# Kernel optimization log

Hardware: AMD Instinct MI355X
Metric: run time of the kernel (lower is better)

Reference implementation:

```python
import jax, jax.numpy as jnp
import numpy as np

B, S, D, H = 2, 2048, 1024, 16
DK = D // H


def setup_inputs() -> dict:
    key = jax.random.key(0)
    ks = jax.random.split(key, 12)
    k_init = 1.0 / np.sqrt(D)  # torch Linear-style uniform bound used in the module
    def lin(kw, kb):
        W = jax.random.uniform(kw, (D, D), jnp.float32, -k_init, k_init)
        b = jax.random.uniform(kb, (D,), jnp.float32, -k_init, k_init)
        return W, b
    Wq, bq = lin(ks[0], ks[1])
    Wk, bk = lin(ks[2], ks[3])
    Wv, bv = lin(ks[4], ks[5])
    Wo, bo = lin(ks[6], ks[7])
    query = jax.random.normal(ks[8], (B, S, D), jnp.float32)
    key_t = jax.random.normal(ks[9], (B, S, D), jnp.float32)
    value = jax.random.normal(ks[10], (B, S, D), jnp.float32)
    # causal mask: 1 where attention allowed, 0 where blocked
    mask = jnp.broadcast_to(jnp.tril(jnp.ones((S, S), jnp.int32)), (B, S, S))
    return {"query": query, "key": key_t, "value": value, "mask": mask,
            "Wq": Wq, "bq": bq, "Wk": Wk, "bk": bk, "Wv": Wv, "bv": bv,
            "Wo": Wo, "bo": bo}


def reference(query, key, value, mask, Wq, bq, Wk, bk, Wv, bv, Wo, bo):
    bs = query.shape[0]
    # projections: torch Linear computes x @ W.T + b
    def proj(x, W, b):
        y = x @ W.T + b                      # [B, S, D]
        return y.reshape(bs, -1, H, DK).transpose(0, 2, 1, 3)  # [B, H, S, DK]
    q = proj(query, Wq, bq)
    k = proj(key, Wk, bk)
    v = proj(value, Wv, bv)
    scale = 1.0 / np.sqrt(DK).astype(np.float32)
    scores = jnp.einsum('bhqd,bhkd->bhqk', q, k) * scale  # [B, H, S, S]
    scores = jnp.where(mask[:, None, :, :] == 0, jnp.float32(-1e9), scores)
    p_attn = jax.nn.softmax(scores, axis=-1)
    # dropout omitted (eval mode / deterministic reference)
    x = jnp.einsum('bhqk,bhkd->bhqd', p_attn, v)          # [B, H, S, DK]
    x = x.transpose(0, 2, 1, 3).reshape(bs, -1, D)        # [B, S, D]
    return x @ Wo.T + bo
```

## Files before the change

### kernel.cpp

```cpp
#include <hip/hip_runtime.h>
#include <hip/hip_bf16.h>
#include <math.h>

#define BB 2
#define SS 2048
#define DD 1024
#define HH 16
#define DKK 64
#define NT (BB * SS)
#define QBLK 128
#define NQT (SS / QBLK)

typedef __attribute__((ext_vector_type(8))) short short8;
typedef __attribute__((ext_vector_type(4))) float f32x4;

#define SWZ(r) ((((r) >> 3) ^ (r)) & 7)

__device__ __forceinline__ unsigned short f2b(float x) {
    __hip_bfloat16 h = __float2bfloat16(x);
    unsigned short u; __builtin_memcpy(&u, &h, 2); return u;
}

__device__ __forceinline__ f32x4 zero4() {
    f32x4 z; z[0] = 0.f; z[1] = 0.f; z[2] = 0.f; z[3] = 0.f; return z;
}

struct CastAll {
    const float* src[7];
    unsigned short* dst[7];
};

__global__ __launch_bounds__(256)
void cast_all(CastAll a) {
    const int tid0 = blockIdx.x * 256 + threadIdx.x;
    const int stride = gridDim.x * 256;
    #pragma unroll
    for (int s = 0; s < 7; ++s) {
        const int n4 = (s < 3) ? (NT * DD / 4) : (DD * DD / 4);
        const float* __restrict__ src = a.src[s];
        unsigned short* __restrict__ dst = a.dst[s];
        for (int i = tid0; i < n4; i += stride) {
            const float4 v = reinterpret_cast<const float4*>(src)[i];
            ushort4 o;
            o.x = f2b(v.x); o.y = f2b(v.y); o.z = f2b(v.z); o.w = f2b(v.w);
            reinterpret_cast<ushort4*>(dst)[i] = o;
        }
    }
}

template <typename OutT>
__device__ __forceinline__ void gemm_body(const unsigned short* __restrict__ A,
                                          const unsigned short* __restrict__ W,
                                          const float* __restrict__ bias,
                                          OutT* __restrict__ C,
                                          int bm, int bn, int N, int K) {
    __shared__ __align__(16) unsigned char sA[128 * 128];
    __shared__ __align__(16) unsigned char sB[128 * 128];

    const int tid = threadIdx.x;
    const int l = tid & 63;
    const int w = tid >> 6;
    const int wr = w >> 1, wc = w & 1;
    const int g = l >> 4, li = l & 15;
    const int lrow = l >> 3;
    const int lcol = (l & 7) * 8;

    f32x4 acc[4][4];
    #pragma unroll
    for (int i = 0; i < 4; ++i)
        #pragma unroll
        for (int jj = 0; jj < 4; ++jj) acc[i][jj] = zero4();

    for (int kt = 0; kt < K; kt += 64) {
        #pragma unroll
        for (int c = 0; c < 4; ++c) {
            const int row0 = w * 32 + c * 8;
            const unsigned short* gA = A + (size_t)(bm + row0 + lrow) * K + kt + lcol;
            __builtin_amdgcn_global_load_lds(
                (const __attribute__((address_space(1))) unsigned int*)gA,
                (__attribute__((address_space(3))) unsigned int*)&sA[row0 * 128],
                16, 0, 0);
            const unsigned short* gB = W + (size_t)(bn + row0 + lrow) * K + kt + lcol;
            __builtin_amdgcn_global_load_lds(
                (const __attribute__((address_space(1))) unsigned int*)gB,
                (__attribute__((address_space(3))) unsigned int*)&sB[row0 * 128],
                16, 0, 0);
        }
        __syncthreads();

        #pragma unroll
        for (int kb = 0; kb < 2; ++kb) {
            const int chb = (g + kb * 4) * 16;
            short8 af[4], bfr[4];
            #pragma unroll
            for (int mi = 0; mi < 4; ++mi)
                af[mi] = *reinterpret_cast<const short8*>(
                    &sA[(wr * 64 + mi * 16 + li) * 128 + chb]);
            #pragma unroll
            for (int ni = 0; ni < 4; ++ni)
                bfr[ni] = *reinterpret_cast<const short8*>(
                    &sB[(wc * 64 + ni * 16 + li) * 128 + chb]);
            #pragma unroll
            for (int mi = 0; mi < 4; ++mi)
                #pragma unroll
                for (int ni = 0; ni < 4; ++ni)
                    acc[mi][ni] = __builtin_amdgcn_mfma_f32_16x16x32_bf16(af[mi], bfr[ni], acc[mi][ni], 0, 0, 0);
        }
        __syncthreads();
    }

    #pragma unroll
    for (int ni = 0; ni < 4; ++ni) {
        const int col = bn + wc * 64 + ni * 16 + li;
        const float bv = bias[col];
        #pragma unroll
        for (int mi = 0; mi < 4; ++mi) {
            const int row0 = bm + wr * 64 + mi * 16 + g * 4;
            #pragma unroll
            for (int r = 0; r < 4; ++r) {
                const float v = acc[mi][ni][r] + bv;
                if constexpr (sizeof(OutT) == 2)
                    C[(size_t)(row0 + r) * N + col] = (OutT)f2b(v);
                else
                    C[(size_t)(row0 + r) * N + col] = (OutT)v;
            }
        }
    }
}

struct QKVArgs {
    const unsigned short* A[3];
    const unsigned short* W[3];
    const float* bias[3];
    unsigned short* C[3];
};

__global__ __launch_bounds__(256)
void gemm_qkv(QKVArgs args) {
    const int bid = blockIdx.x;
    const int i = (bid & 7) * 96 + (bid >> 3);
    const int z = i >> 8;
    const int rem = i & 255;
    const int by = rem >> 3, bx = rem & 7;
    gemm_body<unsigned short>(args.A[z], args.W[z], args.bias[z], args.C[z],
                              by * 128, bx * 128, DD, DD);
}

__global__ __launch_bounds__(256)
void gemm_out(const unsigned short* __restrict__ A, const unsigned short* __restrict__ W,
              const float* __restrict__ bias, float* __restrict__ C) {
    const int bid = blockIdx.x;
    const int i = (bid & 7) * 32 + (bid >> 3);
    const int by = i >> 3, bx = i & 7;
    gemm_body<float>(A, W, bias, C, by * 128, bx * 128, DD, DD);
}

__global__ __launch_bounds__(512)
void attn_mfma(const unsigned short* __restrict__ Q,
               const unsigned short* __restrict__ Kb,
               const unsigned short* __restrict__ Vb,
               unsigned short* __restrict__ X) {
    __shared__ __align__(16) unsigned char sK[64 * 128];
    __shared__ __align__(16) unsigned char sV[64 * 128];
    __shared__ __align__(16) unsigned char sP[8][16 * 128];

    const int bid = blockIdx.x;
    const int j = bid >> 3;
    const int pair = (bid & 7) * 4 + (j >> 4);
    const int qt = (NQT - 1) - (j & 15);
    const int b = pair >> 4, h = pair & 15;

    const int tid = threadIdx.x, l = tid & 63, w = tid >> 6;
    const int g = l >> 4, li = l & 15;
    const int tok0 = b * SS + qt * QBLK;
    const int col0 = h * DKK;
    const float scale = 0.125f;

    short8 qf[2];
    {
        const size_t qrow = (size_t)(tok0 + w * 16 + li) * DD + col0;
        qf[0] = *reinterpret_cast<const short8*>(&Q[qrow + g * 8]);
        qf[1] = *reinterpret_cast<const short8*>(&Q[qrow + 32 + g * 8]);
    }

    f32x4 accO[4];
    #pragma unroll
    for (int i = 0; i < 4; ++i) accO[i] = zero4();
    float m = -INFINITY, lsum = 0.f;
    const int qglob = qt * QBLK + w * 16 + li;
    const int qminw = qt * QBLK + w * 16;
    const int ktmax = 2 * qt + 1;

    for (int kt = 0; kt <= ktmax; ++kt) {
        const int ktok0 = b * SS + kt * 64;

        {
            const int row = tid >> 3, cj = tid & 7;
            const size_t gsrc = (size_t)(ktok0 + row) * DD + col0 + cj * 8;
            const short8 kv8 = *reinterpret_cast<const short8*>(&Kb[gsrc]);
            *reinterpret_cast<short8*>(&sK[row * 128 + ((cj ^ SWZ(row)) << 4)]) = kv8;
            const short8 vv8 = *reinterpret_cast<const short8*>(&Vb[gsrc]);
            #pragma unroll
            for (int jj = 0; jj < 8; ++jj) {
                const int d = cj * 8 + jj;
                *reinterpret_cast<unsigned short*>(
                    &sV[d * 128 + (((row >> 3) ^ SWZ(d)) << 4) + (row & 7) * 2]) =
                    (unsigned short)vv8[jj];
            }
        }
        __syncthreads();

        if (kt * 64 <= qminw + 15) {
            f32x4 accS[4];
            #pragma unroll
            for (int n0 = 0; n0 < 4; ++n0) accS[n0] = zero4();
            #pragma unroll
            for (int n0 = 0; n0 < 4; ++n0) {
                #pragma unroll
                for (int kb = 0; kb < 2; ++kb) {
                    const int row = n0 * 16 + li;
                    const int ch = g + kb * 4;
                    const short8 kf = *reinterpret_cast<const short8*>(
                        &sK[row * 128 + ((ch ^ SWZ(row)) << 4)]);
                    accS[n0] = __builtin_amdgcn_mfma_f32_16x16x32_bf16(kf, qf[kb], accS[n0], 0, 0, 0);
                }
            }

            const bool needMask = (kt * 64 + 63) > qminw;
            float s[16];
            float tmax = -INFINITY;
            #pragma unroll
            for (int n0 = 0; n0 < 4; ++n0)
                #pragma unroll
                for (int r = 0; r < 4; ++r) {
                    float v = accS[n0][r] * scale;
                    if (needMask) {
                        const int kv = kt * 64 + n0 * 16 + g * 4 + r;
                        if (kv > qglob) v = -1e30f;
                    }
                    s[n0 * 4 + r] = v;
                    tmax = fmaxf(tmax, v);
                }
            tmax = fmaxf(tmax, __shfl_xor(tmax, 16));
            tmax = fmaxf(tmax, __shfl_xor(tmax, 32));
            const float mnew = fmaxf(m, tmax);
            const float corr = __expf(m - mnew);
            float psum = 0.f;
            #pragma unroll
            for (int i = 0; i < 16; ++i) { s[i] = __expf(s[i] - mnew); psum += s[i]; }
            psum += __shfl_xor(psum, 16);
            psum += __shfl_xor(psum, 32);
            lsum = lsum * corr + psum;
            m = mnew;

            #pragma unroll
            for (int n0 = 0; n0 < 4; ++n0)
                #pragma unroll
                for (int r = 0; r < 4; ++r) {
                    const int kv = n0 * 16 + g * 4 + r;
                    *reinterpret_cast<unsigned short*>(
                        &sP[w][li * 128 + (((kv >> 3) ^ SWZ(li)) << 4) + (kv & 7) * 2]) =
                        f2b(s[n0 * 4 + r]);
                }

            float corr4[4];
            #pragma unroll
            for (int r = 0; r < 4; ++r) corr4[r] = __shfl(corr, (l & 48) | (g * 4 + r));
            #pragma unroll
            for (int n0d = 0; n0d < 4; ++n0d)
                #pragma unroll
                for (int r = 0; r < 4; ++r) accO[n0d][r] *= corr4[r];

            #pragma unroll
            for (int kb = 0; kb < 2; ++kb) {
                const int ch = g + kb * 4;
                const short8 pf = *reinterpret_cast<const short8*>(
                    &sP[w][li * 128 + ((ch ^ SWZ(li)) << 4)]);
                #pragma unroll
                for (int n0d = 0; n0d < 4; ++n0d) {
                    const int d = n0d * 16 + li;
                    const short8 vf = *reinterpret_cast<const short8*>(
                        &sV[d * 128 + ((ch ^ SWZ(d)) << 4)]);
                    accO[n0d] = __builtin_amdgcn_mfma_f32_16x16x32_bf16(pf, vf, accO[n0d], 0, 0, 0);
                }
            }
        }
        __syncthreads();
    }

    const float invl = 1.f / lsum;
    float inv4[4];
    #pragma unroll
    for (int r = 0; r < 4; ++r) inv4[r] = __shfl(invl, (l & 48) | (g * 4 + r));
    #pragma unroll
    for (int n0d = 0; n0d < 4; ++n0d)
        #pragma unroll
        for (int r = 0; r < 4; ++r) {
            const int row = tok0 + w * 16 + g * 4 + r;
            const int d = n0d * 16 + li;
            X[(size_t)row * DD + col0 + d] = f2b(accO[n0d][r] * inv4[r]);
        }
}

extern "C" void kernel_launch(void* const* d_in, const int* in_sizes, int n_in,
                              void* d_out, int out_size, void* d_ws, size_t ws_size,
                              hipStream_t stream) {
    const float* query = (const float*)d_in[0];
    const float* key   = (const float*)d_in[1];
    const float* value = (const float*)d_in[2];
    const float* Wq = (const float*)d_in[4];
    const float* bq = (const float*)d_in[5];
    const float* Wk = (const float*)d_in[6];
    const float* bk = (const float*)d_in[7];
    const float* Wv = (const float*)d_in[8];
    const float* bv = (const float*)d_in[9];
    const float* Wo = (const float*)d_in[10];
    const float* bo = (const float*)d_in[11];
    float* out = (float*)d_out;

    unsigned short* ws16 = (unsigned short*)d_ws;
    const size_t TOK = (size_t)NT * DD;
    const size_t WSZ = (size_t)DD * DD;
    unsigned short* qb  = ws16;
    unsigned short* kb  = ws16 + TOK;
    unsigned short* vb  = ws16 + 2 * TOK;
    unsigned short* xb  = ws16 + 3 * TOK;
    unsigned short* xqb = ws16 + 4 * TOK;
    unsigned short* xkb = ws16 + 5 * TOK;
    unsigned short* xvb = ws16 + 6 * TOK;
    unsigned short* wqb = ws16 + 7 * TOK;
    unsigned short* wkb = wqb + WSZ;
    unsigned short* wvb = wkb + WSZ;
    unsigned short* wob = wvb + WSZ;

    CastAll ca;
    ca.src[0] = query; ca.dst[0] = xqb;
    ca.src[1] = key;   ca.dst[1] = xkb;
    ca.src[2] = value; ca.dst[2] = xvb;
    ca.src[3] = Wq;    ca.dst[3] = wqb;
    ca.src[4] = Wk;    ca.dst[4] = wkb;
    ca.src[5] = Wv;    ca.dst[5] = wvb;
    ca.src[6] = Wo;    ca.dst[6] = wob;
    cast_all<<<2048, 256, 0, stream>>>(ca);

    QKVArgs args;
    args.A[0] = xqb; args.A[1] = xkb; args.A[2] = xvb;
    args.W[0] = wqb; args.W[1] = wkb; args.W[2] = wvb;
    args.bias[0] = bq; args.bias[1] = bk; args.bias[2] = bv;
    args.C[0] = qb;  args.C[1] = kb;  args.C[2] = vb;
    gemm_qkv<<<768, 256, 0, stream>>>(args);

    attn_mfma<<<512, 512, 0, stream>>>(qb, kb, vb, xb);

    gemm_out<<<256, 256, 0, stream>>>(xb, wob, bo, out);
}
```

Measured before the change: 291.0 us.

## Pair complementary causal query tiles per block to balance attention work

Each attention block now processes two 64-row query tiles, p and 31-p, one per group of four waves. Every block therefore loops over the same number of key tiles, which removes the causal-mask load imbalance between early and late query tiles. The change also packs four bf16 P values into a single 8-byte shared store instead of four scalar stores, and raises wave priority around the MFMA sections. In exchange, waves working on the short tile sit idle through the later key iterations while still taking part in the barriers.

After: 267.5 us. -8.1%, faster.

```diff
diff --git a/kernel.cpp b/kernel.cpp
--- a/kernel.cpp
+++ b/kernel.cpp
@@ -8,10 +8,9 @@
 #define HH 16
 #define DKK 64
 #define NT (BB * SS)
-#define QBLK 128
-#define NQT (SS / QBLK)
 
 typedef __attribute__((ext_vector_type(8))) short short8;
+typedef __attribute__((ext_vector_type(4))) short short4v;
 typedef __attribute__((ext_vector_type(4))) float f32x4;
 
 #define SWZ(r) ((((r) >> 3) ^ (r)) & 7)
@@ -165,20 +164,21 @@
     __shared__ __align__(16) unsigned char sP[8][16 * 128];
 
     const int bid = blockIdx.x;
-    const int j = bid >> 3;
-    const int pair = (bid & 7) * 4 + (j >> 4);
-    const int qt = (NQT - 1) - (j & 15);
-    const int b = pair >> 4, h = pair & 15;
+    const int t = bid >> 3;
+    const int bh = (bid & 7) + 8 * (t & 3);
+    const int p = t >> 2;
+    const int b = bh >> 4, h = bh & 15;
 
     const int tid = threadIdx.x, l = tid & 63, w = tid >> 6;
     const int g = l >> 4, li = l & 15;
-    const int tok0 = b * SS + qt * QBLK;
+    const int jsel = (w < 4) ? p : (31 - p);
+    const int rowb = jsel * 64 + (w & 3) * 16;
     const int col0 = h * DKK;
     const float scale = 0.125f;
 
     short8 qf[2];
     {
-        const size_t qrow = (size_t)(tok0 + w * 16 + li) * DD + col0;
+        const size_t qrow = (size_t)(b * SS + rowb + li) * DD + col0;
         qf[0] = *reinterpret_cast<const short8*>(&Q[qrow + g * 8]);
         qf[1] = *reinterpret_cast<const short8*>(&Q[qrow + 32 + g * 8]);
     }
@@ -187,11 +187,10 @@
     #pragma unroll
     for (int i = 0; i < 4; ++i) accO[i] = zero4();
     float m = -INFINITY, lsum = 0.f;
-    const int qglob = qt * QBLK + w * 16 + li;
-    const int qminw = qt * QBLK + w * 16;
-    const int ktmax = 2 * qt + 1;
-
-    for (int kt = 0; kt <= ktmax; ++kt) {
+    const int qglob = rowb + li;
+    const int nkt = 31 - p;
+
+    for (int kt = 0; kt <= nkt; ++kt) {
         const int ktok0 = b * SS + kt * 64;
 
         {
@@ -210,10 +209,11 @@
         }
         __syncthreads();
 
-        if (kt * 64 <= qminw + 15) {
+        if (kt * 64 <= rowb + 15) {
             f32x4 accS[4];
             #pragma unroll
             for (int n0 = 0; n0 < 4; ++n0) accS[n0] = zero4();
+            __builtin_amdgcn_s_setprio(1);
             #pragma unroll
             for (int n0 = 0; n0 < 4; ++n0) {
                 #pragma unroll
@@ -225,8 +225,9 @@
                     accS[n0] = __builtin_amdgcn_mfma_f32_16x16x32_bf16(kf, qf[kb], accS[n0], 0, 0, 0);
                 }
             }
-
-            const bool needMask = (kt * 64 + 63) > qminw;
+            __builtin_amdgcn_s_setprio(0);
+
+            const bool needMask = (kt * 64 + 63) > rowb;
             float s[16];
             float tmax = -INFINITY;
             #pragma unroll
@@ -254,14 +255,13 @@
             m = mnew;
 
             #pragma unroll
-            for (int n0 = 0; n0 < 4; ++n0)
-                #pragma unroll
-                for (int r = 0; r < 4; ++r) {
-                    const int kv = n0 * 16 + g * 4 + r;
-                    *reinterpret_cast<unsigned short*>(
-                        &sP[w][li * 128 + (((kv >> 3) ^ SWZ(li)) << 4) + (kv & 7) * 2]) =
-                        f2b(s[n0 * 4 + r]);
-                }
+            for (int n0 = 0; n0 < 4; ++n0) {
+                short4v pk;
+                #pragma unroll
+                for (int r = 0; r < 4; ++r) pk[r] = (short)f2b(s[n0 * 4 + r]);
+                *reinterpret_cast<short4v*>(
+                    &sP[w][li * 128 + (((n0 * 2 + (g >> 1)) ^ SWZ(li)) << 4) + (g & 1) * 8]) = pk;
+            }
 
             float corr4[4];
             #pragma unroll
@@ -271,6 +271,7 @@
                 #pragma unroll
                 for (int r = 0; r < 4; ++r) accO[n0d][r] *= corr4[r];
 
+            __builtin_amdgcn_s_setprio(1);
             #pragma unroll
             for (int kb = 0; kb < 2; ++kb) {
                 const int ch = g + kb * 4;
@@ -284,6 +285,7 @@
                     accO[n0d] = __builtin_amdgcn_mfma_f32_16x16x32_bf16(pf, vf, accO[n0d], 0, 0, 0);
                 }
             }
+            __builtin_amdgcn_s_setprio(0);
         }
         __syncthreads();
     }
@@ -296,7 +298,7 @@
     for (int n0d = 0; n0d < 4; ++n0d)
         #pragma unroll
         for (int r = 0; r < 4; ++r) {
-            const int row = tok0 + w * 16 + g * 4 + r;
+            const int row = b * SS + rowb + g * 4 + r;
             const int d = n0d * 16 + li;
             X[(size_t)row * DD + col0 + d] = f2b(accO[n0d][r] * inv4[r]);
         }
```
